# Kernel tuning notes

Measured on AMD Instinct MI355X. Metric: run time of the kernel, lower is better.

The kernel has to match this reference:

```python
import jax, jax.numpy as jnp
import numpy as np

D_MODEL = 1024
N_HEADS = 16
D_HEAD = D_MODEL // N_HEADS


def setup_inputs() -> dict:
    key = jax.random.key(0)
    ks = jax.random.split(key, 7)
    x = jax.random.normal(ks[0], (1, 4096, D_MODEL), dtype=jnp.float32)
    # torch Linear default init ~ U(-1/sqrt(fan_in), 1/sqrt(fan_in)); small randn is fine for a reference
    Wqkv = jax.random.normal(ks[1], (3 * D_MODEL, D_MODEL), dtype=jnp.float32) * (1.0 / np.sqrt(D_MODEL))
    bqkv = jax.random.normal(ks[2], (3 * D_MODEL,), dtype=jnp.float32) * 0.01
    Wo = jax.random.normal(ks[3], (D_MODEL, D_MODEL), dtype=jnp.float32) * (1.0 / np.sqrt(D_MODEL))
    bo = jax.random.normal(ks[4], (D_MODEL,), dtype=jnp.float32) * 0.01
    wq = jnp.ones((D_HEAD,), dtype=jnp.float32)
    wk = jnp.ones((D_HEAD,), dtype=jnp.float32)
    return {"x": x, "Wqkv": Wqkv, "bqkv": bqkv, "Wo": Wo, "bo": bo, "wq": wq, "wk": wk}


def _rmsnorm(x, w):
    # matches RMSNormRef: mean of squares over last dim, eps added to mean before sqrt
    xf = x.astype(jnp.float32)
    rms = jnp.mean(xf * xf, axis=-1, keepdims=True)
    return (xf / jnp.sqrt(rms + 1e-6) * w.astype(jnp.float32)).astype(x.dtype)


def reference(x, Wqkv, bqkv, Wo, bo, wq, wk):
    b, s, d = x.shape
    qkv = x @ Wqkv.T + bqkv                       # [b, s, 3d]
    q, k, v = jnp.split(qkv, 3, axis=-1)
    q = q.reshape(b, s, N_HEADS, D_HEAD)
    k = k.reshape(b, s, N_HEADS, D_HEAD)
    v = v.reshape(b, s, N_HEADS, D_HEAD)
    q = _rmsnorm(q, wq)
    k = _rmsnorm(k, wk)
    # NOTE: original applies NO 1/sqrt(d_head) scaling and NO causal mask
    qf = q.astype(jnp.float32)
    kf = k.astype(jnp.float32)
    vf = v.astype(jnp.float32)
    attn = jnp.einsum('bqhd,bkhd->bhqk', qf, kf)  # [b, h, s, s] fp32 scores
    attn = jax.nn.softmax(attn, axis=-1)
    z = jnp.einsum('bhqk,bkhd->bqhd', attn, vf).astype(x.dtype)
    z = z.reshape(b, s, d)
    return z @ Wo.T + bo
```

## Files before the change

kernel.cpp:

```cpp
#include <hip/hip_runtime.h>
#include <hip/hip_bf16.h>

typedef __bf16 bf16;
typedef bf16 bf16x8 __attribute__((ext_vector_type(8)));
typedef bf16 bf16x4 __attribute__((ext_vector_type(4)));
typedef float f32x4 __attribute__((ext_vector_type(4)));
typedef float f32x16 __attribute__((ext_vector_type(16)));
typedef unsigned int u32;
typedef u32 u32x4 __attribute__((ext_vector_type(4)));

static constexpr int SEQ    = 4096;
static constexpr int DMODEL = 1024;
static constexpr int NHEADS = 16;
static constexpr int DHEAD  = 64;
static constexpr int QKV3   = 3 * DMODEL;
static constexpr float SMAX = 64.0f;
static constexpr float LOG2E = 1.44269504088896341f;

__device__ inline void gld16(const bf16* g, bf16* l) {
    __builtin_amdgcn_global_load_lds(
        (const __attribute__((address_space(1))) void*)g,
        (__attribute__((address_space(3))) void*)l, 16, 0, 0);
}

__device__ inline bf16x8 load8(const float* src) {
    float4 a = *(const float4*)(src);
    float4 b = *(const float4*)(src + 4);
    bf16x8 r;
    r[0] = (bf16)a.x; r[1] = (bf16)a.y; r[2] = (bf16)a.z; r[3] = (bf16)a.w;
    r[4] = (bf16)b.x; r[5] = (bf16)b.y; r[6] = (bf16)b.z; r[7] = (bf16)b.w;
    return r;
}

__device__ inline f32x16 zero16() {
    f32x16 r;
#pragma unroll
    for (int i = 0; i < 16; ++i) r[i] = 0.f;
    return r;
}

static constexpr size_t NX = (size_t)SEQ * DMODEL;
static constexpr size_t NW = (size_t)QKV3 * DMODEL;
static constexpr size_t NO = (size_t)DMODEL * DMODEL;

__global__ __launch_bounds__(256)
void cvt_all(const float* __restrict__ x, const float* __restrict__ Wqkv,
             const float* __restrict__ Wo, bf16* __restrict__ outbase) {
    const size_t e = ((size_t)blockIdx.x * 256 + threadIdx.x) * 8;
    const float* src;
    if (e < NX)            src = x + e;
    else if (e < NX + NW)  src = Wqkv + (e - NX);
    else                   src = Wo + (e - NX - NW);
    *(bf16x8*)(outbase + e) = load8(src);
}

__global__ __launch_bounds__(256)
void gemm_qkv(const bf16* __restrict__ A, const bf16* __restrict__ W,
              const float* __restrict__ bias, const float* __restrict__ wq,
              const float* __restrict__ wk, bf16* __restrict__ qkv,
              bf16* __restrict__ Vt) {
    __shared__ __align__(16) bf16 As[128 * 64];
    __shared__ __align__(16) bf16 Ws[128 * 64];
    const int tid  = threadIdx.x;
    const int wave = tid >> 6;
    const int ll   = tid & 15;
    const int quad = (tid & 63) >> 4;
    const int wm   = (wave >> 1) * 64;
    const int wn   = (wave & 1) * 64;
    const int m0 = blockIdx.y * 128;
    const int n0 = blockIdx.x * 128;

    f32x4 acc[4][4];
#pragma unroll
    for (int i = 0; i < 4; ++i)
#pragma unroll
        for (int j = 0; j < 4; ++j) acc[i][j] = (f32x4){0.f, 0.f, 0.f, 0.f};

    for (int k0 = 0; k0 < DMODEL; k0 += 64) {
        __syncthreads();
#pragma unroll
        for (int i = 0; i < 4; ++i) {
            const int idx = i * 256 + tid;
            const int row = idx >> 3;
            const int c   = (idx & 7) ^ (row & 7);
            gld16(&A[(size_t)(m0 + row) * DMODEL + k0 + c * 8], As + idx * 8);
            gld16(&W[(size_t)(n0 + row) * DMODEL + k0 + c * 8], Ws + idx * 8);
        }
        __syncthreads();
#pragma unroll
        for (int kk = 0; kk < 2; ++kk) {
            bf16x8 af[4], bfr[4];
#pragma unroll
            for (int mi = 0; mi < 4; ++mi) {
                const int row = wm + mi * 16 + ll;
                const int p   = (kk * 4 + quad) ^ (ll & 7);
                af[mi] = *(const bf16x8*)(As + (row * 8 + p) * 8);
            }
#pragma unroll
            for (int ni = 0; ni < 4; ++ni) {
                const int row = wn + ni * 16 + ll;
                const int p   = (kk * 4 + quad) ^ (ll & 7);
                bfr[ni] = *(const bf16x8*)(Ws + (row * 8 + p) * 8);
            }
#pragma unroll
            for (int mi = 0; mi < 4; ++mi)
#pragma unroll
                for (int ni = 0; ni < 4; ++ni)
                    acc[mi][ni] = __builtin_amdgcn_mfma_f32_16x16x32_bf16(
                        af[mi], bfr[ni], acc[mi][ni], 0, 0, 0);
        }
    }

    float bvn[4];
#pragma unroll
    for (int ni = 0; ni < 4; ++ni) bvn[ni] = bias[n0 + wn + ni * 16 + ll];

    const int sect = (n0 + wn) >> 10;
    if (sect < 2) {
        const float* wv = sect ? wk : wq;
        float wvl[4];
#pragma unroll
        for (int ni = 0; ni < 4; ++ni) wvl[ni] = wv[ni * 16 + ll];
#pragma unroll
        for (int mi = 0; mi < 4; ++mi)
#pragma unroll
            for (int r = 0; r < 4; ++r) {
                float xf[4];
                float ss = 0.f;
#pragma unroll
                for (int ni = 0; ni < 4; ++ni) {
                    xf[ni] = (float)(bf16)(acc[mi][ni][r] + bvn[ni]);
                    ss += xf[ni] * xf[ni];
                }
#pragma unroll
                for (int off = 1; off < 16; off <<= 1) ss += __shfl_xor(ss, off);
                const float scale = rsqrtf(ss * (1.0f / 64.0f) + 1e-6f);
                const int row = m0 + wm + mi * 16 + quad * 4 + r;
#pragma unroll
                for (int ni = 0; ni < 4; ++ni)
                    qkv[(size_t)row * QKV3 + n0 + wn + ni * 16 + ll] =
                        (bf16)(xf[ni] * scale * wvl[ni]);
            }
    } else {
        const int h = (n0 + wn - 2 * DMODEL) >> 6;
#pragma unroll
        for (int mi = 0; mi < 4; ++mi) {
            const int kv = m0 + wm + mi * 16 + quad * 4;
#pragma unroll
            for (int ni = 0; ni < 4; ++ni) {
                bf16x4 vv;
#pragma unroll
                for (int r = 0; r < 4; ++r) vv[r] = (bf16)(acc[mi][ni][r] + bvn[ni]);
                *(bf16x4*)(Vt + (size_t)(h * DHEAD + ni * 16 + ll) * SEQ + kv) = vv;
            }
        }
    }
}

__global__ __launch_bounds__(256)
void gemm_out(const bf16* __restrict__ A, const bf16* __restrict__ W,
              const float* __restrict__ bias, float* __restrict__ C) {
    __shared__ __align__(16) bf16 As[128 * 64];
    __shared__ __align__(16) bf16 Ws[64 * 64];
    const int tid  = threadIdx.x;
    const int wave = tid >> 6;
    const int ll   = tid & 15;
    const int quad = (tid & 63) >> 4;
    const int m0 = blockIdx.y * 128;
    const int n0 = blockIdx.x * 64;

    f32x4 acc[2][4];
#pragma unroll
    for (int i = 0; i < 2; ++i)
#pragma unroll
        for (int j = 0; j < 4; ++j) acc[i][j] = (f32x4){0.f, 0.f, 0.f, 0.f};

    for (int k0 = 0; k0 < DMODEL; k0 += 64) {
        __syncthreads();
#pragma unroll
        for (int i = 0; i < 4; ++i) {
            const int idx = i * 256 + tid;
            const int row = idx >> 3;
            const int c   = (idx & 7) ^ (row & 7);
            gld16(&A[(size_t)(m0 + row) * DMODEL + k0 + c * 8], As + idx * 8);
        }
#pragma unroll
        for (int i = 0; i < 2; ++i) {
            const int idx = i * 256 + tid;
            const int row = idx >> 3;
            const int c   = (idx & 7) ^ (row & 7);
            gld16(&W[(size_t)(n0 + row) * DMODEL + k0 + c * 8], Ws + idx * 8);
        }
        __syncthreads();
#pragma unroll
        for (int kk = 0; kk < 2; ++kk) {
            bf16x8 af[2], bfr[4];
#pragma unroll
            for (int mi = 0; mi < 2; ++mi) {
                const int row = wave * 32 + mi * 16 + ll;
                const int p   = (kk * 4 + quad) ^ (ll & 7);
                af[mi] = *(const bf16x8*)(As + (row * 8 + p) * 8);
            }
#pragma unroll
            for (int ni = 0; ni < 4; ++ni) {
                const int row = ni * 16 + ll;
                const int p   = (kk * 4 + quad) ^ (ll & 7);
                bfr[ni] = *(const bf16x8*)(Ws + (row * 8 + p) * 8);
            }
#pragma unroll
            for (int mi = 0; mi < 2; ++mi)
#pragma unroll
                for (int ni = 0; ni < 4; ++ni)
                    acc[mi][ni] = __builtin_amdgcn_mfma_f32_16x16x32_bf16(
                        af[mi], bfr[ni], acc[mi][ni], 0, 0, 0);
        }
    }
#pragma unroll
    for (int ni = 0; ni < 4; ++ni) {
        const int col = n0 + ni * 16 + ll;
        const float bv = bias[col];
#pragma unroll
        for (int mi = 0; mi < 2; ++mi)
#pragma unroll
            for (int r = 0; r < 4; ++r) {
                const int row = m0 + wave * 32 + mi * 16 + quad * 4 + r;
                C[(size_t)row * DMODEL + col] = acc[mi][ni][r] + bv;
            }
    }
}

template<int NSPLIT>
__global__ __launch_bounds__(256, 2)
void attn_fwd(const bf16* __restrict__ qkv, const bf16* __restrict__ Vt,
              bf16* __restrict__ z, float* __restrict__ opf,
              float* __restrict__ lsum) {
    constexpr bool PARTIAL = (NSPLIT > 1);
    __shared__ __align__(16) bf16 KV[2][2][128 * 64];
    float (*Os)[32][36] = (float(*)[32][36])(&KV[0][0][0]);
    bf16* Qs = &KV[0][0][0];

    const int tid  = threadIdx.x;
    const int wave = tid >> 6;
    const int lane = tid & 63;
    const int l31  = lane & 31;
    const int hh   = lane >> 5;
    const int l7   = lane & 7;
    const int head = blockIdx.x;
    const int q0   = blockIdx.y * 256;
    const int half = PARTIAL ? blockIdx.z : 0;
    const int kvlen = SEQ / NSPLIT;
    const int kvbeg = half * kvlen;
    const int nt    = kvlen / 128;

    const bf16* kbase  = qkv + DMODEL + head * DHEAD;
    const bf16* vtbase = Vt + (size_t)head * DHEAD * SEQ;

    auto stage_kv = [&](int buf, int kv0) {
#pragma unroll
        for (int i = 0; i < 4; ++i) {
            const int idx = i * 256 + tid;
            {
                const int row = idx >> 3;
                const int c   = (idx & 7) ^ (row & 7);
                gld16(kbase + (size_t)(kv0 + row) * QKV3 + c * 8,
                      &KV[buf][0][0] + idx * 8);
            }
            {
                const int row = idx >> 4;
                const int c   = (idx & 15) ^ (row & 15);
                gld16(vtbase + (size_t)row * SEQ + kv0 + c * 8,
                      &KV[buf][1][0] + idx * 8);
            }
        }
    };

#pragma unroll
    for (int i = 0; i < 8; ++i) {
        const int idx = i * 256 + tid;
        const int row = idx >> 3;
        const int c   = (idx & 7) ^ (row & 7);
        gld16(qkv + (size_t)(q0 + row) * QKV3 + head * DHEAD + c * 8, Qs + idx * 8);
    }
    __syncthreads();
    bf16x8 qf[4][2];
#pragma unroll
    for (int kd = 0; kd < 4; ++kd)
#pragma unroll
        for (int qs = 0; qs < 2; ++qs) {
            const int row = wave * 64 + qs * 32 + l31;
            qf[kd][qs] = *(const bf16x8*)(Qs + (row * 8 + ((kd * 2 + hh) ^ l7)) * 8);
        }
    __syncthreads();
    stage_kv(0, kvbeg);
    __syncthreads();

    f32x16 o[2][2];
    o[0][0] = zero16(); o[0][1] = zero16();
    o[1][0] = zero16(); o[1][1] = zero16();
    float lpa[2][4] = {{0.f, 0.f, 0.f, 0.f}, {0.f, 0.f, 0.f, 0.f}};

    int cur = 0;
    for (int t = 0; t < nt; ++t) {
        if (t + 1 < nt) stage_kv(cur ^ 1, kvbeg + (t + 1) * 128);
        const bf16* Ks  = &KV[cur][0][0];
        const bf16* VTs = &KV[cur][1][0];

#pragma unroll
        for (int kvt = 0; kvt < 4; ++kvt) {
            f32x16 st0 = zero16(), st1 = zero16();
            __builtin_amdgcn_s_setprio(1);
#pragma unroll
            for (int kd = 0; kd < 4; ++kd) {
                bf16x8 kf = *(const bf16x8*)(
                    Ks + ((kvt * 32 + l31) * 8 + ((kd * 2 + hh) ^ l7)) * 8);
                st0 = __builtin_amdgcn_mfma_f32_32x32x16_bf16(kf, qf[kd][0], st0, 0, 0, 0);
                st1 = __builtin_amdgcn_mfma_f32_32x32x16_bf16(kf, qf[kd][1], st1, 0, 0, 0);
            }
            __builtin_amdgcn_s_setprio(0);

            float pf0[16], pf1[16];
#pragma unroll
            for (int r = 0; r < 16; ++r)
                pf0[r] = __builtin_amdgcn_exp2f(
                    __builtin_fmaf(st0[r], LOG2E, -SMAX * LOG2E));
#pragma unroll
            for (int r = 0; r < 16; ++r)
                pf1[r] = __builtin_amdgcn_exp2f(
                    __builtin_fmaf(st1[r], LOG2E, -SMAX * LOG2E));
#pragma unroll
            for (int r = 0; r < 16; ++r) lpa[0][r & 3] += pf0[r];
#pragma unroll
            for (int r = 0; r < 16; ++r) lpa[1][r & 3] += pf1[r];

#pragma unroll
            for (int cc = 0; cc < 2; ++cc) {
                u32 a1, b1, a2, b2, a3, b3, a4, b4;
                asm("v_cvt_pk_bf16_f32 %0, %1, %2" : "=v"(a1) : "v"(pf0[8 * cc + 0]), "v"(pf0[8 * cc + 1]));
                asm("v_cvt_pk_bf16_f32 %0, %1, %2" : "=v"(b1) : "v"(pf0[8 * cc + 4]), "v"(pf0[8 * cc + 5]));
                asm("v_cvt_pk_bf16_f32 %0, %1, %2" : "=v"(a2) : "v"(pf0[8 * cc + 2]), "v"(pf0[8 * cc + 3]));
                asm("v_cvt_pk_bf16_f32 %0, %1, %2" : "=v"(b2) : "v"(pf0[8 * cc + 6]), "v"(pf0[8 * cc + 7]));
                asm("v_permlane32_swap_b32 %0, %1" : "+v"(a1), "+v"(b1));
                asm("v_permlane32_swap_b32 %0, %1" : "+v"(a2), "+v"(b2));
                asm("v_cvt_pk_bf16_f32 %0, %1, %2" : "=v"(a3) : "v"(pf1[8 * cc + 0]), "v"(pf1[8 * cc + 1]));
                asm("v_cvt_pk_bf16_f32 %0, %1, %2" : "=v"(b3) : "v"(pf1[8 * cc + 4]), "v"(pf1[8 * cc + 5]));
                asm("v_cvt_pk_bf16_f32 %0, %1, %2" : "=v"(a4) : "v"(pf1[8 * cc + 2]), "v"(pf1[8 * cc + 3]));
                asm("v_cvt_pk_bf16_f32 %0, %1, %2" : "=v"(b4) : "v"(pf1[8 * cc + 6]), "v"(pf1[8 * cc + 7]));
                asm("v_permlane32_swap_b32 %0, %1" : "+v"(a3), "+v"(b3));
                asm("v_permlane32_swap_b32 %0, %1" : "+v"(a4), "+v"(b4));
                u32x4 w0, w1;
                w0[0] = a1; w0[1] = a2; w0[2] = b1; w0[3] = b2;
                w1[0] = a3; w1[1] = a4; w1[2] = b3; w1[3] = b4;
                const bf16x8 bp0 = *(const bf16x8*)&w0;
                const bf16x8 bp1 = *(const bf16x8*)&w1;
                const int ck = (kvt * 2 + cc) * 2 + hh;
                __builtin_amdgcn_s_setprio(1);
#pragma unroll
                for (int dt = 0; dt < 2; ++dt) {
                    const int d = dt * 32 + l31;
                    bf16x8 vf = *(const bf16x8*)(
                        VTs + (d * 16 + (ck ^ (d & 15))) * 8);
                    o[dt][0] = __builtin_amdgcn_mfma_f32_32x32x16_bf16(vf, bp0, o[dt][0], 0, 0, 0);
                    o[dt][1] = __builtin_amdgcn_mfma_f32_32x32x16_bf16(vf, bp1, o[dt][1], 0, 0, 0);
                }
                __builtin_amdgcn_s_setprio(0);
            }
        }
        __syncthreads();
        cur ^= 1;
    }

#pragma unroll
    for (int qs = 0; qs < 2; ++qs) {
        float lp = (lpa[qs][0] + lpa[qs][1]) + (lpa[qs][2] + lpa[qs][3]);
        lp += __shfl_xor(lp, 32);
        const int qrow = q0 + wave * 64 + qs * 32 + l31;
        if (PARTIAL) {
            if (lane < 32) lsum[((size_t)half * SEQ + qrow) * NHEADS + head] = lp;
        }
        const float inv = PARTIAL ? 1.0f : 1.0f / lp;

#pragma unroll
        for (int dt = 0; dt < 2; ++dt) {
#pragma unroll
            for (int r = 0; r < 16; ++r) {
                const int dl = (r & 3) + 8 * (r >> 2) + 4 * hh;
                Os[wave][l31][dl] = o[dt][qs][r] * inv;
            }
#pragma unroll
            for (int it = 0; it < 4; ++it) {
                const int qr  = it * 8 + (lane >> 3);
                const int dl2 = (lane & 7) * 4;
                const f32x4 v = *(const f32x4*)(&Os[wave][qr][dl2]);
                const int row = q0 + wave * 64 + qs * 32 + qr;
                const int col = head * DHEAD + dt * 32 + dl2;
                if (PARTIAL) {
                    *(f32x4*)(opf + ((size_t)half * SEQ + row) * DMODEL + col) = v;
                } else {
                    bf16x4 ov;
                    ov[0] = (bf16)v[0]; ov[1] = (bf16)v[1];
                    ov[2] = (bf16)v[2]; ov[3] = (bf16)v[3];
                    *(bf16x4*)(z + (size_t)row * DMODEL + col) = ov;
                }
            }
        }
    }
}

template<int NS>
__global__ __launch_bounds__(256)
void combine_halves(const float* __restrict__ opf, const float* __restrict__ lsum,
                    bf16* __restrict__ z) {
    const int row = blockIdx.x;
    const int c   = threadIdx.x * 4;
    const int head = c >> 6;
    float l = 0.f;
#pragma unroll
    for (int s = 0; s < NS; ++s)
        l += lsum[((size_t)s * SEQ + row) * NHEADS + head];
    float4 acc = {0.f, 0.f, 0.f, 0.f};
#pragma unroll
    for (int s = 0; s < NS; ++s) {
        const float4 ov = *(const float4*)(opf + ((size_t)s * SEQ + row) * DMODEL + c);
        acc.x += ov.x; acc.y += ov.y; acc.z += ov.z; acc.w += ov.w;
    }
    bf16x4 out;
    out[0] = (bf16)(acc.x / l);
    out[1] = (bf16)(acc.y / l);
    out[2] = (bf16)(acc.z / l);
    out[3] = (bf16)(acc.w / l);
    *(bf16x4*)(z + (size_t)row * DMODEL + c) = out;
}

extern "C" void kernel_launch(void* const* d_in, const int* in_sizes, int n_in,
                              void* d_out, int out_size, void* d_ws, size_t ws_size,
                              hipStream_t stream) {
    const float* x    = (const float*)d_in[0];
    const float* Wqkv = (const float*)d_in[1];
    const float* bqkv = (const float*)d_in[2];
    const float* Wo   = (const float*)d_in[3];
    const float* bo   = (const float*)d_in[4];
    const float* wq   = (const float*)d_in[5];
    const float* wk   = (const float*)d_in[6];
    float* out = (float*)d_out;

    bf16* qkv  = (bf16*)d_ws;
    bf16* z    = qkv + (size_t)SEQ * QKV3;
    bf16* Vt   = z + (size_t)SEQ * DMODEL;
    bf16* xb   = Vt + (size_t)NHEADS * DHEAD * SEQ;
    bf16* Wqb  = xb + NX;
    bf16* Wob  = Wqb + NW;
    bf16* endb = Wob + NO;
    float* opf  = (float*)endb;
    float* lsum2 = opf + (size_t)2 * SEQ * DMODEL;
    const size_t need2 = (size_t)((char*)(lsum2 + (size_t)2 * SEQ * NHEADS) - (char*)d_ws);

    cvt_all<<<dim3((NX + NW + NO) / 2048), 256, 0, stream>>>(x, Wqkv, Wo, xb);

    gemm_qkv<<<dim3(QKV3 / 128, SEQ / 128), 256, 0, stream>>>(
        xb, Wqb, bqkv, wq, wk, qkv, Vt);

    if (ws_size >= need2) {
        attn_fwd<2><<<dim3(NHEADS, SEQ / 256, 2), 256, 0, stream>>>(
            qkv, Vt, z, opf, lsum2);
        combine_halves<2><<<dim3(SEQ), 256, 0, stream>>>(opf, lsum2, z);
    } else {
        attn_fwd<1><<<dim3(NHEADS, SEQ / 256, 1), 256, 0, stream>>>(
            qkv, Vt, z, nullptr, nullptr);
    }

    gemm_out<<<dim3(DMODEL / 64, SEQ / 128), 256, 0, stream>>>(z, Wob, bo, out);
}
```

Baseline: 230.5 us.

## Enlarge QKV GEMM tile to 256x256 with double-buffered LDS pipeline

The QKV projection GEMM moves from 128x128 tiles with 4 waves to 256x256 tiles with 8 waves. It double-buffers the LDS staging so global-to-LDS loads for the next K-step are issued in halves, interleaved with MFMA phases, and s_setprio raises priority around the MFMA bursts. The aim is more operand reuse per tile and hiding global load latency behind compute. In exchange it uses 128KB of LDS per block, which may limit occupancy, and the grid shrinks to 192 blocks, which can underfill the device's 256 CUs.

Measured after the change: 227.6 us. About the same (-1.2%).

```diff
diff --git a/kernel.cpp b/kernel.cpp
--- a/kernel.cpp
+++ b/kernel.cpp
@@ -54,75 +54,103 @@
     *(bf16x8*)(outbase + e) = load8(src);
 }
 
-__global__ __launch_bounds__(256)
+__global__ __launch_bounds__(512, 2)
 void gemm_qkv(const bf16* __restrict__ A, const bf16* __restrict__ W,
               const float* __restrict__ bias, const float* __restrict__ wq,
               const float* __restrict__ wk, bf16* __restrict__ qkv,
               bf16* __restrict__ Vt) {
-    __shared__ __align__(16) bf16 As[128 * 64];
-    __shared__ __align__(16) bf16 Ws[128 * 64];
+    __shared__ __align__(16) bf16 As[2][256 * 64];
+    __shared__ __align__(16) bf16 Ws[2][256 * 64];
     const int tid  = threadIdx.x;
     const int wave = tid >> 6;
-    const int ll   = tid & 15;
-    const int quad = (tid & 63) >> 4;
-    const int wm   = (wave >> 1) * 64;
-    const int wn   = (wave & 1) * 64;
-    const int m0 = blockIdx.y * 128;
-    const int n0 = blockIdx.x * 128;
-
-    f32x4 acc[4][4];
-#pragma unroll
-    for (int i = 0; i < 4; ++i)
+    const int lane = tid & 63;
+    const int ll   = lane & 15;
+    const int quad = lane >> 4;
+    const int wr   = wave >> 2;
+    const int wc   = wave & 3;
+    const int m0 = blockIdx.y * 256;
+    const int n0 = blockIdx.x * 256;
+    constexpr int NT = DMODEL / 64;
+
+    f32x4 acc[8][4];
+#pragma unroll
+    for (int i = 0; i < 8; ++i)
 #pragma unroll
         for (int j = 0; j < 4; ++j) acc[i][j] = (f32x4){0.f, 0.f, 0.f, 0.f};
 
-    for (int k0 = 0; k0 < DMODEL; k0 += 64) {
-        __syncthreads();
-#pragma unroll
-        for (int i = 0; i < 4; ++i) {
-            const int idx = i * 256 + tid;
+    auto stage_half = [&](int buf, int k0, int h) {
+#pragma unroll
+        for (int j = 2 * h; j < 2 * h + 2; ++j) {
+            const int idx = j * 512 + tid;
             const int row = idx >> 3;
             const int c   = (idx & 7) ^ (row & 7);
-            gld16(&A[(size_t)(m0 + row) * DMODEL + k0 + c * 8], As + idx * 8);
-            gld16(&W[(size_t)(n0 + row) * DMODEL + k0 + c * 8], Ws + idx * 8);
-        }
-        __syncthreads();
-#pragma unroll
-        for (int kk = 0; kk < 2; ++kk) {
-            bf16x8 af[4], bfr[4];
-#pragma unroll
-            for (int mi = 0; mi < 4; ++mi) {
-                const int row = wm + mi * 16 + ll;
+            gld16(&A[(size_t)(m0 + row) * DMODEL + k0 + c * 8], &As[buf][0] + idx * 8);
+            gld16(&W[(size_t)(n0 + row) * DMODEL + k0 + c * 8], &Ws[buf][0] + idx * 8);
+        }
+    };
+
+    stage_half(0, 0, 0);
+    stage_half(0, 0, 1);
+    asm volatile("s_waitcnt vmcnt(0)" ::: "memory");
+    __builtin_amdgcn_s_barrier();
+
+    bf16x8 bfr[4];
+    for (int t = 0; t < NT; ++t) {
+        const int buf = t & 1;
+        const bf16* Ab = &As[buf][0];
+        const bf16* Wb = &Ws[buf][0];
+#pragma unroll
+        for (int ph = 0; ph < 4; ++ph) {
+            const int kk = ph >> 1;
+            const int mh = ph & 1;
+            bf16x8 af[4];
+#pragma unroll
+            for (int i = 0; i < 4; ++i) {
+                const int row = wr * 128 + (mh * 4 + i) * 16 + ll;
                 const int p   = (kk * 4 + quad) ^ (ll & 7);
-                af[mi] = *(const bf16x8*)(As + (row * 8 + p) * 8);
-            }
-#pragma unroll
-            for (int ni = 0; ni < 4; ++ni) {
-                const int row = wn + ni * 16 + ll;
-                const int p   = (kk * 4 + quad) ^ (ll & 7);
-                bfr[ni] = *(const bf16x8*)(Ws + (row * 8 + p) * 8);
-            }
-#pragma unroll
-            for (int mi = 0; mi < 4; ++mi)
+                af[i] = *(const bf16x8*)(Ab + (row * 8 + p) * 8);
+            }
+            if (mh == 0) {
+#pragma unroll
+                for (int ni = 0; ni < 4; ++ni) {
+                    const int row = wc * 64 + ni * 16 + ll;
+                    const int p   = (kk * 4 + quad) ^ (ll & 7);
+                    bfr[ni] = *(const bf16x8*)(Wb + (row * 8 + p) * 8);
+                }
+            }
+            if (ph < 2 && t + 1 < NT) stage_half(buf ^ 1, (t + 1) * 64, ph);
+
+            __builtin_amdgcn_s_barrier();
+            __builtin_amdgcn_s_setprio(1);
+#pragma unroll
+            for (int i = 0; i < 4; ++i)
 #pragma unroll
                 for (int ni = 0; ni < 4; ++ni)
-                    acc[mi][ni] = __builtin_amdgcn_mfma_f32_16x16x32_bf16(
-                        af[mi], bfr[ni], acc[mi][ni], 0, 0, 0);
-        }
-    }
-
+                    acc[mh * 4 + i][ni] = __builtin_amdgcn_mfma_f32_16x16x32_bf16(
+                        af[i], bfr[ni], acc[mh * 4 + i][ni], 0, 0, 0);
+            __builtin_amdgcn_s_setprio(0);
+            if (ph < 3) {
+                __builtin_amdgcn_s_barrier();
+            } else {
+                if (t + 1 < NT) asm volatile("s_waitcnt vmcnt(0)" ::: "memory");
+                __builtin_amdgcn_s_barrier();
+            }
+        }
+    }
+
+    const int ncol0 = n0 + wc * 64;
     float bvn[4];
 #pragma unroll
-    for (int ni = 0; ni < 4; ++ni) bvn[ni] = bias[n0 + wn + ni * 16 + ll];
-
-    const int sect = (n0 + wn) >> 10;
+    for (int ni = 0; ni < 4; ++ni) bvn[ni] = bias[ncol0 + ni * 16 + ll];
+
+    const int sect = ncol0 >> 10;
     if (sect < 2) {
         const float* wv = sect ? wk : wq;
         float wvl[4];
 #pragma unroll
         for (int ni = 0; ni < 4; ++ni) wvl[ni] = wv[ni * 16 + ll];
 #pragma unroll
-        for (int mi = 0; mi < 4; ++mi)
+        for (int mi = 0; mi < 8; ++mi)
 #pragma unroll
             for (int r = 0; r < 4; ++r) {
                 float xf[4];
@@ -135,17 +163,17 @@
 #pragma unroll
                 for (int off = 1; off < 16; off <<= 1) ss += __shfl_xor(ss, off);
                 const float scale = rsqrtf(ss * (1.0f / 64.0f) + 1e-6f);
-                const int row = m0 + wm + mi * 16 + quad * 4 + r;
+                const int row = m0 + wr * 128 + mi * 16 + quad * 4 + r;
 #pragma unroll
                 for (int ni = 0; ni < 4; ++ni)
-                    qkv[(size_t)row * QKV3 + n0 + wn + ni * 16 + ll] =
+                    qkv[(size_t)row * QKV3 + ncol0 + ni * 16 + ll] =
                         (bf16)(xf[ni] * scale * wvl[ni]);
             }
     } else {
-        const int h = (n0 + wn - 2 * DMODEL) >> 6;
-#pragma unroll
-        for (int mi = 0; mi < 4; ++mi) {
-            const int kv = m0 + wm + mi * 16 + quad * 4;
+        const int h = (ncol0 - 2 * DMODEL) >> 6;
+#pragma unroll
+        for (int mi = 0; mi < 8; ++mi) {
+            const int kv = m0 + wr * 128 + mi * 16 + quad * 4;
 #pragma unroll
             for (int ni = 0; ni < 4; ++ni) {
                 bf16x4 vv;
@@ -456,7 +484,7 @@
 
     cvt_all<<<dim3((NX + NW + NO) / 2048), 256, 0, stream>>>(x, Wqkv, Wo, xb);
 
-    gemm_qkv<<<dim3(QKV3 / 128, SEQ / 128), 256, 0, stream>>>(
+    gemm_qkv<<<dim3(QKV3 / 256, SEQ / 256), 512, 0, stream>>>(
         xb, Wqb, bqkv, wq, wk, qkv, Vt);
 
     if (ws_size >= need2) {
```
